# Optimization experiments

Measured on AMD Instinct MI355X. Metric: run time of the kernel, lower is better.

## Reference

```python
import jax, jax.numpy as jnp
import numpy as np

# layer dims of the hard-coded linear chain (torch Linear: y = x @ W.T + b)
_DIMS = [784, 69, 31, 10, 10, 10, 10, 10, 10, 10]


def setup_inputs() -> dict:
    key = jax.random.key(0)
    ks = jax.random.split(key, 1 + 2 * 9)
    inp = {"x": jax.random.normal(ks[0], (65536, 784), dtype=jnp.float32)}
    for i in range(9):
        fan_in, fan_out = _DIMS[i], _DIMS[i + 1]
        bound = 1.0 / np.sqrt(fan_in)
        inp[f"W{i}"] = jax.random.uniform(ks[1 + 2 * i], (fan_out, fan_in), dtype=jnp.float32, minval=-bound, maxval=bound)
        inp[f"b{i}"] = jax.random.uniform(ks[2 + 2 * i], (fan_out,), dtype=jnp.float32, minval=-bound, maxval=bound)
    return inp


def reference(x, W0, b0, W1, b1, W2, b2, W3, b3, W4, b4, W5, b5, W6, b6, W7, b7, W8, b8):
    Ws = [W0, W1, W2, W3, W4, W5, W6, W7, W8]
    bs = [b0, b1, b2, b3, b4, b5, b6, b7, b8]
    for W, b in zip(Ws, bs):
        x = x @ W.T + b  # [B, out]
    return x
```

## Files before the change

### kernel.cpp

```cpp
#include <hip/hip_runtime.h>


__global__ void prep_collapse(
    const float* __restrict__ W1, const float* __restrict__ b1,
    const float* __restrict__ W2, const float* __restrict__ b2,
    const float* __restrict__ W3, const float* __restrict__ b3,
    const float* __restrict__ W4, const float* __restrict__ b4,
    const float* __restrict__ W5, const float* __restrict__ b5,
    const float* __restrict__ W6, const float* __restrict__ b6,
    const float* __restrict__ W7, const float* __restrict__ b7,
    const float* __restrict__ W8, const float* __restrict__ b8,
    const float* __restrict__ b0,
    float* __restrict__ S8out, float* __restrict__ beff)
{
    __shared__ float Sa[31 * 69], Sb[31 * 69];
    __shared__ float da[31], db[31];
    const int t = threadIdx.x;
    const int nt = blockDim.x;

    for (int i = t; i < 31 * 69; i += nt) Sa[i] = W1[i];
    for (int i = t; i < 31; i += nt) da[i] = b1[i];
    __syncthreads();

    for (int i = t; i < 10 * 69; i += nt) {
        int o = i / 69, c = i - o * 69;
        float s = 0.f;
        for (int k = 0; k < 31; k++) s += W2[o * 31 + k] * Sa[k * 69 + c];
        Sb[i] = s;
    }
    for (int i = t; i < 10; i += nt) {
        float s = b2[i];
        for (int k = 0; k < 31; k++) s += W2[i * 31 + k] * da[k];
        db[i] = s;
    }
    __syncthreads();

    const float* Wk[6] = { W3, W4, W5, W6, W7, W8 };
    const float* bk[6] = { b3, b4, b5, b6, b7, b8 };
    int src = 1;
    for (int st = 0; st < 6; st++) {
        const float* W = Wk[st];
        const float* bb = bk[st];
        float* S  = src ? Sb : Sa;
        float* D  = src ? Sa : Sb;
        float* dd = src ? db : da;
        float* dn = src ? da : db;
        for (int i = t; i < 10 * 69; i += nt) {
            int o = i / 69, c = i - o * 69;
            float s = 0.f;
            for (int k = 0; k < 10; k++) s += W[o * 10 + k] * S[k * 69 + c];
            D[i] = s;
        }
        for (int i = t; i < 10; i += nt) {
            float s = bb[i];
            for (int k = 0; k < 10; k++) s += W[i * 10 + k] * dd[k];
            dn[i] = s;
        }
        __syncthreads();
        src ^= 1;
    }

    float* S  = src ? Sb : Sa;
    float* dd = src ? db : da;
    for (int i = t; i < 690; i += nt) S8out[i] = S[i];
    for (int i = t; i < 10; i += nt) {
        float s = dd[i];
        for (int k = 0; k < 69; k++) s += S[i * 69 + k] * b0[k];
        beff[i] = s;
    }
}

__global__ void prep_fold0(const float* __restrict__ W0,
                           const float* __restrict__ S8,
                           float* __restrict__ Wt)
{
    int idx = blockIdx.x * blockDim.x + threadIdx.x;
    if (idx >= 7840) return;
    int o = idx / 784, j = idx - o * 784;
    float s = 0.f;
    for (int k = 0; k < 69; k++) s += S8[o * 69 + k] * W0[k * 784 + j];
    Wt[j * 10 + o] = s;
}


#define LOADG(dst, g)                                               \
    _Pragma("unroll")                                               \
    for (int i = 0; i < 7; i++)                                     \
        dst[i] = *(const float4*)(xp + (g) * 28 + i * 4);

#define COMP(src, g)                                                \
    _Pragma("unroll")                                               \
    for (int i = 0; i < 7; i++) {                                   \
        const float* w = wp + ((g) * 28 + i * 4) * 10;              \
        _Pragma("unroll")                                           \
        for (int o = 0; o < 10; o++) acc[o] = fmaf(src[i].x, w[o],      acc[o]); \
        _Pragma("unroll")                                           \
        for (int o = 0; o < 10; o++) acc[o] = fmaf(src[i].y, w[10 + o], acc[o]); \
        _Pragma("unroll")                                           \
        for (int o = 0; o < 10; o++) acc[o] = fmaf(src[i].z, w[20 + o], acc[o]); \
        _Pragma("unroll")                                           \
        for (int o = 0; o < 10; o++) acc[o] = fmaf(src[i].w, w[30 + o], acc[o]); \
    }

__global__ __launch_bounds__(256, 4) void linear_main(
    const float* __restrict__ x, const float* __restrict__ Wt,
    const float* __restrict__ beff, float* __restrict__ out)
{
    __shared__ float part[3 * 64 * 10];
    const int t = threadIdx.x;
    const int lane = t & 63;
    const int q = __builtin_amdgcn_readfirstlane(t >> 6);
    const long row = (long)blockIdx.x * 64 + lane;

    const float* xp = x + row * 784 + q * 196;
    const float* __restrict__ wp = Wt + q * 1960;

    float acc[10];
#pragma unroll
    for (int o = 0; o < 10; o++) acc[o] = 0.f;

    float4 A[7], Bv[7];
    LOADG(A, 0)
    LOADG(Bv, 1) COMP(A, 0)
    LOADG(A, 2)  COMP(Bv, 1)
    LOADG(Bv, 3) COMP(A, 2)
    LOADG(A, 4)  COMP(Bv, 3)
    LOADG(Bv, 5) COMP(A, 4)
    LOADG(A, 6)  COMP(Bv, 5)
    COMP(A, 6)

    if (q != 0) {
#pragma unroll
        for (int o = 0; o < 10; o++) part[(q - 1) * 640 + lane * 10 + o] = acc[o];
    }
    __syncthreads();
    if (q == 0) {
#pragma unroll
        for (int w = 0; w < 3; w++)
#pragma unroll
            for (int o = 0; o < 10; o++) acc[o] += part[w * 640 + lane * 10 + o];
        float* op = out + row * 10;
#pragma unroll
        for (int o = 0; o < 10; o += 2)
            *(float2*)(op + o) = make_float2(acc[o] + beff[o], acc[o + 1] + beff[o + 1]);
    }
}

extern "C" void kernel_launch(void* const* d_in, const int* in_sizes, int n_in,
                              void* d_out, int out_size, void* d_ws, size_t ws_size,
                              hipStream_t stream) {
    const float* x  = (const float*)d_in[0];
    const float* W0 = (const float*)d_in[1];
    const float* b0 = (const float*)d_in[2];
    const float* W1 = (const float*)d_in[3];
    const float* b1 = (const float*)d_in[4];
    const float* W2 = (const float*)d_in[5];
    const float* b2 = (const float*)d_in[6];
    const float* W3 = (const float*)d_in[7];
    const float* b3 = (const float*)d_in[8];
    const float* W4 = (const float*)d_in[9];
    const float* b4 = (const float*)d_in[10];
    const float* W5 = (const float*)d_in[11];
    const float* b5 = (const float*)d_in[12];
    const float* W6 = (const float*)d_in[13];
    const float* b6 = (const float*)d_in[14];
    const float* W7 = (const float*)d_in[15];
    const float* b7 = (const float*)d_in[16];
    const float* W8 = (const float*)d_in[17];
    const float* b8 = (const float*)d_in[18];

    float* ws   = (float*)d_ws;
    float* Wt   = ws;
    float* beff = ws + 7840;
    float* S8   = ws + 7856;

    float* out = (float*)d_out;
    const int B = in_sizes[0] / 784;

    prep_collapse<<<1, 256, 0, stream>>>(W1, b1, W2, b2, W3, b3, W4, b4,
                                         W5, b5, W6, b6, W7, b7, W8, b8,
                                         b0, S8, beff);
    prep_fold0<<<31, 256, 0, stream>>>(W0, S8, Wt);
    linear_main<<<B / 64, 256, 0, stream>>>(x, Wt, beff, out);
}
```

Baseline: 370.1 us.

## Coalesce x loads via swizzled LDS staging and split K across blocks with atomics

Each block is now a single wave handling one K-quarter of 64 rows. The wave cooperatively loads contiguous chunks of x into a swizzled LDS tile, then each lane reads its own row from LDS. This replaces strided per-lane row loads with coalesced global reads. Partial sums from the four K-quarter blocks are combined with global atomicAdd into an output zeroed by a memset, which replaces the intra-block LDS reduction. This adds atomic traffic and an extra memset launch, and it relies on wave-lockstep ordering for LDS without explicit barriers.

```diff
diff --git a/kernel.cpp b/kernel.cpp
--- a/kernel.cpp
+++ b/kernel.cpp
@@ -83,67 +83,72 @@
 }
 
 
-#define LOADG(dst, g)                                               \
-    _Pragma("unroll")                                               \
-    for (int i = 0; i < 7; i++)                                     \
-        dst[i] = *(const float4*)(xp + (g) * 28 + i * 4);
-
-#define COMP(src, g)                                                \
-    _Pragma("unroll")                                               \
-    for (int i = 0; i < 7; i++) {                                   \
-        const float* w = wp + ((g) * 28 + i * 4) * 10;              \
-        _Pragma("unroll")                                           \
-        for (int o = 0; o < 10; o++) acc[o] = fmaf(src[i].x, w[o],      acc[o]); \
-        _Pragma("unroll")                                           \
-        for (int o = 0; o < 10; o++) acc[o] = fmaf(src[i].y, w[10 + o], acc[o]); \
-        _Pragma("unroll")                                           \
-        for (int o = 0; o < 10; o++) acc[o] = fmaf(src[i].z, w[20 + o], acc[o]); \
-        _Pragma("unroll")                                           \
-        for (int o = 0; o < 10; o++) acc[o] = fmaf(src[i].w, w[30 + o], acc[o]); \
-    }
-
-__global__ __launch_bounds__(256, 4) void linear_main(
+__global__ __launch_bounds__(64, 4) void linear_main(
     const float* __restrict__ x, const float* __restrict__ Wt,
     const float* __restrict__ beff, float* __restrict__ out)
 {
-    __shared__ float part[3 * 64 * 10];
-    const int t = threadIdx.x;
-    const int lane = t & 63;
-    const int q = __builtin_amdgcn_readfirstlane(t >> 6);
-    const long row = (long)blockIdx.x * 64 + lane;
+    __shared__ float xs[64 * 32];
+    const int l  = threadIdx.x;
+    const int rb = blockIdx.x >> 2;
+    const int q  = blockIdx.x & 3;
+    const long row0 = (long)rb * 64;
+    const float* xq = x + row0 * 784 + q * 196;
+    const float* __restrict__ wq = Wt + q * 1960;
 
-    const float* xp = x + row * 784 + q * 196;
-    const float* __restrict__ wp = Wt + q * 1960;
+    int srow[7], sj[7];
+#pragma unroll
+    for (int i = 0; i < 7; i++) {
+        int g = i * 64 + l;
+        srow[i] = g / 7;
+        sj[i]   = g - 7 * srow[i];
+    }
 
     float acc[10];
 #pragma unroll
     for (int o = 0; o < 10; o++) acc[o] = 0.f;
 
-    float4 A[7], Bv[7];
-    LOADG(A, 0)
-    LOADG(Bv, 1) COMP(A, 0)
-    LOADG(A, 2)  COMP(Bv, 1)
-    LOADG(Bv, 3) COMP(A, 2)
-    LOADG(A, 4)  COMP(Bv, 3)
-    LOADG(Bv, 5) COMP(A, 4)
-    LOADG(A, 6)  COMP(Bv, 5)
-    COMP(A, 6)
+    float4 pf[7];
+#pragma unroll
+    for (int i = 0; i < 7; i++)
+        pf[i] = *(const float4*)(xq + srow[i] * 784 + 4 * sj[i]);
+#pragma unroll
+    for (int i = 0; i < 7; i++)
+        *(float4*)&xs[srow[i] * 32 + 4 * ((sj[i] + srow[i]) & 7)] = pf[i];
 
-    if (q != 0) {
+    for (int c = 0; c < 7; c++) {
+        if (c < 6) {
 #pragma unroll
-        for (int o = 0; o < 10; o++) part[(q - 1) * 640 + lane * 10 + o] = acc[o];
+            for (int i = 0; i < 7; i++)
+                pf[i] = *(const float4*)(xq + srow[i] * 784 + (c + 1) * 28 + 4 * sj[i]);
+        }
+        const float* wc = wq + c * 280;
+#pragma unroll
+        for (int j4 = 0; j4 < 7; j4++) {
+            float4 xv = *(const float4*)&xs[l * 32 + 4 * ((j4 + l) & 7)];
+            const float* w = wc + j4 * 40;
+#pragma unroll
+            for (int o = 0; o < 10; o++) acc[o] = fmaf(xv.x, w[o],      acc[o]);
+#pragma unroll
+            for (int o = 0; o < 10; o++) acc[o] = fmaf(xv.y, w[10 + o], acc[o]);
+#pragma unroll
+            for (int o = 0; o < 10; o++) acc[o] = fmaf(xv.z, w[20 + o], acc[o]);
+#pragma unroll
+            for (int o = 0; o < 10; o++) acc[o] = fmaf(xv.w, w[30 + o], acc[o]);
+        }
+        if (c < 6) {
+#pragma unroll
+            for (int i = 0; i < 7; i++)
+                *(float4*)&xs[srow[i] * 32 + 4 * ((sj[i] + srow[i]) & 7)] = pf[i];
+        }
     }
-    __syncthreads();
-    if (q == 0) {
+
+    if (q == 3) {
 #pragma unroll
-        for (int w = 0; w < 3; w++)
+        for (int o = 0; o < 10; o++) acc[o] += beff[o];
+    }
+    float* op = out + (row0 + l) * 10;
 #pragma unroll
-            for (int o = 0; o < 10; o++) acc[o] += part[w * 640 + lane * 10 + o];
-        float* op = out + row * 10;
-#pragma unroll
-        for (int o = 0; o < 10; o += 2)
-            *(float2*)(op + o) = make_float2(acc[o] + beff[o], acc[o + 1] + beff[o + 1]);
-    }
+    for (int o = 0; o < 10; o++) atomicAdd(op + o, acc[o]);
 }
 
 extern "C" void kernel_launch(void* const* d_in, const int* in_sizes, int n_in,
@@ -181,5 +186,6 @@
                                          W5, b5, W6, b6, W7, b7, W8, b8,
                                          b0, S8, beff);
     prep_fold0<<<31, 256, 0, stream>>>(W0, S8, Wt);
-    linear_main<<<B / 64, 256, 0, stream>>>(x, Wt, beff, out);
+    hipMemsetAsync(out, 0, (size_t)out_size * sizeof(float), stream);
+    linear_main<<<(B / 64) * 4, 64, 0, stream>>>(x, Wt, beff, out);
 }
```

After: 454.5 us. 22.8% more time.

## Restructure main GEMV: 8 threads per row, LDS-staged padded weights, shuffle reduction

Applied to the files above, without the earlier changes.

The fold kernel now writes the collapsed 784x10 weight in a padded interleaved layout: groups of 4 input columns, each holding 10 float4 plus one pad float4. The main kernel stages this whole table into LDS once per block. Eight consecutive threads now cooperate on one row, each reading a contiguous float4 per step, and partial sums are combined with xor shuffles instead of an LDS partial-sum exchange. The goal is more coalesced x loads and cheap, conflict-avoiding weight reads. In exchange, each block reloads about 35 KB of weights and only a single float4 is prefetched at a time, which may limit latency hiding.

```diff
diff --git a/kernel.cpp b/kernel.cpp
--- a/kernel.cpp
+++ b/kernel.cpp
@@ -72,77 +72,76 @@
 
 __global__ void prep_fold0(const float* __restrict__ W0,
                            const float* __restrict__ S8,
-                           float* __restrict__ Wt)
+                           float* __restrict__ Wt2)
 {
     int idx = blockIdx.x * blockDim.x + threadIdx.x;
-    if (idx >= 7840) return;
-    int o = idx / 784, j = idx - o * 784;
-    float s = 0.f;
-    for (int k = 0; k < 69; k++) s += S8[o * 69 + k] * W0[k * 784 + j];
-    Wt[j * 10 + o] = s;
+    if (idx >= 8800) return;
+    int j4 = idx / 44, rem = idx - j4 * 44;
+    float val = 0.f;
+    if (rem < 40) {
+        int o = rem >> 2, k = rem & 3, j = j4 * 4 + k;
+        if (j < 784) {
+            for (int u = 0; u < 69; u++) val += S8[o * 69 + u] * W0[u * 784 + j];
+        }
+    }
+    Wt2[idx] = val;
 }
 
 
-#define LOADG(dst, g)                                               \
-    _Pragma("unroll")                                               \
-    for (int i = 0; i < 7; i++)                                     \
-        dst[i] = *(const float4*)(xp + (g) * 28 + i * 4);
-
-#define COMP(src, g)                                                \
-    _Pragma("unroll")                                               \
-    for (int i = 0; i < 7; i++) {                                   \
-        const float* w = wp + ((g) * 28 + i * 4) * 10;              \
-        _Pragma("unroll")                                           \
-        for (int o = 0; o < 10; o++) acc[o] = fmaf(src[i].x, w[o],      acc[o]); \
-        _Pragma("unroll")                                           \
-        for (int o = 0; o < 10; o++) acc[o] = fmaf(src[i].y, w[10 + o], acc[o]); \
-        _Pragma("unroll")                                           \
-        for (int o = 0; o < 10; o++) acc[o] = fmaf(src[i].z, w[20 + o], acc[o]); \
-        _Pragma("unroll")                                           \
-        for (int o = 0; o < 10; o++) acc[o] = fmaf(src[i].w, w[30 + o], acc[o]); \
-    }
-
-__global__ __launch_bounds__(256, 4) void linear_main(
-    const float* __restrict__ x, const float* __restrict__ Wt,
+__global__ __launch_bounds__(512, 8) void linear_main(
+    const float* __restrict__ x, const float* __restrict__ Wt2,
     const float* __restrict__ beff, float* __restrict__ out)
 {
-    __shared__ float part[3 * 64 * 10];
+    __shared__ float4 wlds[2200];
     const int t = threadIdx.x;
-    const int lane = t & 63;
-    const int q = __builtin_amdgcn_readfirstlane(t >> 6);
-    const long row = (long)blockIdx.x * 64 + lane;
+    const int s = t & 7;
+    const long row = (long)blockIdx.x * 64 + (t >> 3);
+    const float* xrow = x + row * 784;
 
-    const float* xp = x + row * 784 + q * 196;
-    const float* __restrict__ wp = Wt + q * 1960;
+    {
+        const float4* wg = (const float4*)Wt2;
+        for (int i = t; i < 2200; i += 512) wlds[i] = wg[i];
+    }
 
     float acc[10];
 #pragma unroll
     for (int o = 0; o < 10; o++) acc[o] = 0.f;
 
-    float4 A[7], Bv[7];
-    LOADG(A, 0)
-    LOADG(Bv, 1) COMP(A, 0)
-    LOADG(A, 2)  COMP(Bv, 1)
-    LOADG(Bv, 3) COMP(A, 2)
-    LOADG(A, 4)  COMP(Bv, 3)
-    LOADG(Bv, 5) COMP(A, 4)
-    LOADG(A, 6)  COMP(Bv, 5)
-    COMP(A, 6)
+    float4 xv = *(const float4*)(xrow + s * 4);
+    __syncthreads();
 
-    if (q != 0) {
+    for (int jb = 0; jb < 25; jb++) {
+        float4 xc = xv;
+        if (jb < 24) {
+            int jn = (jb + 1) * 32 + s * 4;
+            jn = jn > 780 ? 780 : jn;
+            xv = *(const float4*)(xrow + jn);
+        }
+        const float4* wrow = &wlds[(jb * 8 + s) * 11];
 #pragma unroll
-        for (int o = 0; o < 10; o++) part[(q - 1) * 640 + lane * 10 + o] = acc[o];
+        for (int o = 0; o < 10; o++) {
+            float4 wv = wrow[o];
+            acc[o] = fmaf(xc.x, wv.x, acc[o]);
+            acc[o] = fmaf(xc.y, wv.y, acc[o]);
+            acc[o] = fmaf(xc.z, wv.z, acc[o]);
+            acc[o] = fmaf(xc.w, wv.w, acc[o]);
+        }
     }
-    __syncthreads();
-    if (q == 0) {
+
 #pragma unroll
-        for (int w = 0; w < 3; w++)
+    for (int m = 1; m < 8; m <<= 1)
 #pragma unroll
-            for (int o = 0; o < 10; o++) acc[o] += part[w * 640 + lane * 10 + o];
-        float* op = out + row * 10;
+        for (int o = 0; o < 10; o++) acc[o] += __shfl_xor(acc[o], m, 64);
+
+    if (s < 5) {
+        float lo = 0.f, hi = 0.f;
 #pragma unroll
-        for (int o = 0; o < 10; o += 2)
-            *(float2*)(op + o) = make_float2(acc[o] + beff[o], acc[o + 1] + beff[o + 1]);
+        for (int o = 0; o < 5; o++) {
+            if (s == o) { lo = acc[2 * o]; hi = acc[2 * o + 1]; }
+        }
+        lo += beff[s * 2];
+        hi += beff[s * 2 + 1];
+        *(float2*)(out + row * 10 + s * 2) = make_float2(lo, hi);
     }
 }
 
@@ -170,9 +169,9 @@
     const float* b8 = (const float*)d_in[18];
 
     float* ws   = (float*)d_ws;
-    float* Wt   = ws;
-    float* beff = ws + 7840;
-    float* S8   = ws + 7856;
+    float* Wt2  = ws;
+    float* beff = ws + 8800;
+    float* S8   = ws + 8816;
 
     float* out = (float*)d_out;
     const int B = in_sizes[0] / 784;
@@ -180,6 +179,6 @@
     prep_collapse<<<1, 256, 0, stream>>>(W1, b1, W2, b2, W3, b3, W4, b4,
                                          W5, b5, W6, b6, W7, b7, W8, b8,
                                          b0, S8, beff);
-    prep_fold0<<<31, 256, 0, stream>>>(W0, S8, Wt);
-    linear_main<<<B / 64, 256, 0, stream>>>(x, Wt, beff, out);
+    prep_fold0<<<35, 256, 0, stream>>>(W0, S8, Wt2);
+    linear_main<<<B / 64, 512, 0, stream>>>(x, Wt2, beff, out);
 }
```

Result: faster. 351.3 us (-5.1%).
